# Optimization experiments

Measured on AMD Instinct MI355X. Metric: run time of the kernel, lower is better.

## Reference

```python
import jax, jax.numpy as jnp
import numpy as np

B, S, L, F = 32, 48, 64, 256


def setup_inputs() -> dict:
    key = jax.random.key(0)
    ks = jax.random.split(key, 7)
    return {
        "features": jax.random.normal(ks[0], (B, S, L, F), dtype=jnp.float32),
        "src_locs": jax.random.normal(ks[1], (B, L, 2), dtype=jnp.float32),
        "tar_locs": jax.random.normal(ks[2], (B, 2), dtype=jnp.float32),
        "W1": jax.random.normal(ks[3], (F, F), dtype=jnp.float32) * (1.0 / np.sqrt(F)),
        "b1": jax.random.normal(ks[4], (F,), dtype=jnp.float32) * 0.02,
        "W2": jax.random.normal(ks[5], (F, 1), dtype=jnp.float32) * (1.0 / np.sqrt(F)),
        "b2": jax.random.normal(ks[6], (1,), dtype=jnp.float32) * 0.02,
    }


def reference(features, src_locs, tar_locs, W1, b1, W2, b2):
    # features: (B, S, L, F); src_locs: (B, L, 2); tar_locs: (B, 2)
    # MLP score: Linear(F,F) + ReLU + Linear(F,1) + ReLU -> (B, S, L, 1)
    attn = jax.nn.relu(jnp.einsum('bslf,fg->bslg', features, W1) + b1)
    attn = jax.nn.relu(jnp.einsum('bslf,fo->bslo', attn, W2) + b2)  # (B,S,L,1)
    # inverse-distance weights over stations: (B, L)
    dists = jnp.sqrt(jnp.sum((src_locs - tar_locs[:, None, :]) ** 2, axis=-1))
    inv_dists = 1.0 / dists  # (B, L)
    # broadcast to (B, 1, L, 1), softmax over src_length axis (axis=2)
    attn_scores = jax.nn.softmax(attn * inv_dists[:, None, :, None], axis=2)
    # weighted sum over stations -> (B, S, F)
    return jnp.sum(features * attn_scores, axis=2)
```

## Files before the change

kernel.cpp:

```cpp
#include <hip/hip_runtime.h>
#include <hip/hip_fp16.h>
#include <math.h>

typedef _Float16 half8 __attribute__((ext_vector_type(8)));
typedef float floatx4 __attribute__((ext_vector_type(4)));

#define BB 32
#define SS 48
#define LL 64
#define FF 256

#define WAVE_BARRIER() do {                                          \
    asm volatile("s_waitcnt lgkmcnt(0)" ::: "memory");               \
    __builtin_amdgcn_s_barrier();                                    \
    asm volatile("" ::: "memory");                                   \
} while (0)

#define ISSUE_FENCE() asm volatile("" ::: "memory")

template <int CTRL>
__device__ __forceinline__ float dpp_add(float x) {
    int y = __builtin_amdgcn_update_dpp(0, __float_as_int(x), CTRL, 0xF, 0xF, true);
    return x + __int_as_float(y);
}
template <int CTRL>
__device__ __forceinline__ float dpp_max(float x) {
    int y = __builtin_amdgcn_update_dpp(0, __float_as_int(x), CTRL, 0xF, 0xF, true);
    return fmaxf(x, __int_as_float(y));
}
__device__ __forceinline__ float row16_sum(float x) {
    x = dpp_add<0xB1>(x);
    x = dpp_add<0x4E>(x);
    x = dpp_add<0x124>(x);
    x = dpp_add<0x128>(x);
    return x;
}
__device__ __forceinline__ float row16_max(float x) {
    x = dpp_max<0xB1>(x);
    x = dpp_max<0x4E>(x);
    x = dpp_max<0x124>(x);
    x = dpp_max<0x128>(x);
    return x;
}

__global__ __launch_bounds__(256) void prep_w(const float* __restrict__ W1,
                                              _Float16* __restrict__ whi) {
    int idx = blockIdx.x * 256 + threadIdx.x;
    int j    = idx & 7;
    int lane = (idx >> 3) & 63;
    int nt   = (idx >> 9) & 15;
    int kt   = idx >> 13;
    int k = kt * 32 + ((lane >> 4) & 3) * 8 + j;
    int n = nt * 16 + (lane & 15);
    whi[idx] = (_Float16)W1[k * FF + n];
}

__global__ __launch_bounds__(512, 6) void ida_mfma(
    const float* __restrict__ features,
    const float* __restrict__ src_locs,
    const float* __restrict__ tar_locs,
    const _Float16* __restrict__ whi,
    const float* __restrict__ b1,
    const float* __restrict__ W2,
    const float* __restrict__ b2,
    float* __restrict__ out)
{
    __shared__ _Float16 Ahi[16384];
    __shared__ float SP[8 * LL];

    const int t    = threadIdx.x;
    const int w    = t >> 6;
    const int lane = t & 63;
    const int quad = lane >> 4;
    const int l16  = lane & 15;
    const int bs   = blockIdx.x;
    const int b    = bs / SS;

    const float* Xg = features + (size_t)bs * (LL * FF);

    float sx = src_locs[(b * LL + lane) * 2 + 0];
    float sy = src_locs[(b * LL + lane) * 2 + 1];
    float tx = tar_locs[b * 2 + 0];
    float ty = tar_locs[b * 2 + 1];
    float b2v = b2[0];
    float b1v[2], w2v[2];
    #pragma unroll
    for (int ntl = 0; ntl < 2; ++ntl) {
        int n = (w * 2 + ntl) * 16 + l16;
        b1v[ntl] = b1[n];
        w2v[ntl] = W2[n];
    }
    ISSUE_FENCE();

    float4 araw[8];
    #pragma unroll
    for (int it = 0; it < 4; ++it) {
        int G   = it * 8 + w;
        int row = (G >> 3) * 16 + l16;
        int cb  = (G & 7) * 32 + quad * 8;
        const float4* p = (const float4*)(Xg + row * FF + cb);
        araw[2 * it + 0] = p[0];
        araw[2 * it + 1] = p[1];
    }
    ISSUE_FENCE();

    half8 bh[2], nbh[2];
    #pragma unroll
    for (int ntl = 0; ntl < 2; ++ntl) {
        size_t off = ((size_t)(0 * 16 + (w * 2 + ntl)) * 64 + lane) * 8;
        bh[ntl] = *((const half8*)(whi + off));
    }
    ISSUE_FENCE();

    #pragma unroll
    for (int it = 0; it < 4; ++it) {
        int G = it * 8 + w;
        float4 x0 = araw[2 * it + 0], x1 = araw[2 * it + 1];
        float xs[8] = {x0.x, x0.y, x0.z, x0.w, x1.x, x1.y, x1.z, x1.w};
        half8 hi;
        #pragma unroll
        for (int j = 0; j < 8; ++j) hi[j] = (_Float16)xs[j];
        *((half8*)&Ahi[(G * 64 + lane) * 8]) = hi;
    }

    WAVE_BARRIER();

    floatx4 acc[4][2] = {};

    #pragma unroll
    for (int kt = 0; kt < 8; ++kt) {
        if (kt < 7) {
            #pragma unroll
            for (int ntl = 0; ntl < 2; ++ntl) {
                size_t off = ((size_t)((kt + 1) * 16 + (w * 2 + ntl)) * 64 + lane) * 8;
                nbh[ntl] = *((const half8*)(whi + off));
            }
        }
        #pragma unroll
        for (int mt = 0; mt < 4; ++mt) {
            half8 ahi = *((half8*)&Ahi[((mt * 8 + kt) * 64 + lane) * 8]);
            #pragma unroll
            for (int ntl = 0; ntl < 2; ++ntl)
                acc[mt][ntl] = __builtin_amdgcn_mfma_f32_16x16x32_f16(ahi, bh[ntl], acc[mt][ntl], 0, 0, 0);
        }
        if (kt < 7) { bh[0] = nbh[0]; bh[1] = nbh[1]; }
    }

    #pragma unroll
    for (int mt = 0; mt < 4; ++mt) {
        #pragma unroll
        for (int r = 0; r < 4; ++r) {
            float p = 0.f;
            #pragma unroll
            for (int ntl = 0; ntl < 2; ++ntl) {
                float h = fmaxf(acc[mt][ntl][r] + b1v[ntl], 0.f);
                p = fmaf(h, w2v[ntl], p);
            }
            p = row16_sum(p);
            if (l16 == 0) SP[w * LL + mt * 16 + quad * 4 + r] = p;
        }
    }

    WAVE_BARRIER();

    float s = SP[0 * LL + lane] + SP[1 * LL + lane] + SP[2 * LL + lane] + SP[3 * LL + lane]
            + SP[4 * LL + lane] + SP[5 * LL + lane] + SP[6 * LL + lane] + SP[7 * LL + lane] + b2v;
    float score = fmaxf(s, 0.f);
    float dxv = sx - tx, dyv = sy - ty;
    float inv_d = 1.0f / sqrtf(dxv * dxv + dyv * dyv);
    float logit = score * inv_d;
    float m = row16_max(logit);
    m = fmaxf(m, __shfl_xor(m, 16));
    m = fmaxf(m, __shfl_xor(m, 32));
    float e = __expf(logit - m);
    float se = row16_sum(e);
    se += __shfl_xor(se, 16);
    se += __shfl_xor(se, 32);
    float wgt = e / se;

    float o8[8] = {0.f, 0.f, 0.f, 0.f, 0.f, 0.f, 0.f, 0.f};
    #pragma unroll
    for (int it = 0; it < 4; ++it) {
        float wr = __shfl(wgt, it * 16 + l16);
        half8 hv = *((half8*)&Ahi[((it * 8 + w) * 64 + lane) * 8]);
        #pragma unroll
        for (int j = 0; j < 8; ++j)
            o8[j] = fmaf((float)hv[j], wr, o8[j]);
    }
    #pragma unroll
    for (int j = 0; j < 8; ++j)
        o8[j] = row16_sum(o8[j]);
    if (l16 == 0) {
        float* op = out + (size_t)bs * FF + w * 32 + quad * 8;
        float4 s0 = {o8[0], o8[1], o8[2], o8[3]};
        float4 s1 = {o8[4], o8[5], o8[6], o8[7]};
        *((float4*)op) = s0;
        *((float4*)(op + 4)) = s1;
    }
}

extern "C" void kernel_launch(void* const* d_in, const int* in_sizes, int n_in,
                              void* d_out, int out_size, void* d_ws, size_t ws_size,
                              hipStream_t stream) {
    const float* features = (const float*)d_in[0];
    const float* src_locs = (const float*)d_in[1];
    const float* tar_locs = (const float*)d_in[2];
    const float* W1       = (const float*)d_in[3];
    const float* b1       = (const float*)d_in[4];
    const float* W2       = (const float*)d_in[5];
    const float* b2       = (const float*)d_in[6];
    float* out = (float*)d_out;

    _Float16* whi = (_Float16*)d_ws;

    prep_w<<<dim3(FF * FF / 256), dim3(256), 0, stream>>>(W1, whi);
    ida_mfma<<<dim3(BB * SS), dim3(512), 0, stream>>>(
        features, src_locs, tar_locs, whi, b1, W2, b2, out);
}
```

Baseline: 171.9 us.

## Process three slices per block with register prefetch and double-buffered LDS

Each block now handles three consecutive (b,s) slices instead of one, shrinking the grid by a factor of three. While the MFMA stage of the current slice runs, the next slice's features are loaded into registers, and a two-entry LDS buffer lets the conversion of the next slice proceed without waiting for the current one to be fully consumed. The W1 fragment prefetch becomes a three-deep ring that loads two k-tiles ahead. The cost is twice the LDS per block, a lower occupancy hint, and fewer blocks to spread across the CUs.

```diff
diff --git a/kernel.cpp b/kernel.cpp
--- a/kernel.cpp
+++ b/kernel.cpp
@@ -9,6 +9,8 @@
 #define SS 48
 #define LL 64
 #define FF 256
+#define NSLICE 3
+#define NBLK ((BB * SS) / NSLICE)
 
 #define WAVE_BARRIER() do {                                          \
     asm volatile("s_waitcnt lgkmcnt(0)" ::: "memory");               \
@@ -55,7 +57,7 @@
     whi[idx] = (_Float16)W1[k * FF + n];
 }
 
-__global__ __launch_bounds__(512, 6) void ida_mfma(
+__global__ __launch_bounds__(512, 4) void ida_mfma(
     const float* __restrict__ features,
     const float* __restrict__ src_locs,
     const float* __restrict__ tar_locs,
@@ -65,7 +67,7 @@
     const float* __restrict__ b2,
     float* __restrict__ out)
 {
-    __shared__ _Float16 Ahi[16384];
+    __shared__ _Float16 Ahi[2][16384];
     __shared__ float SP[8 * LL];
 
     const int t    = threadIdx.x;
@@ -73,16 +75,8 @@
     const int lane = t & 63;
     const int quad = lane >> 4;
     const int l16  = lane & 15;
-    const int bs   = blockIdx.x;
-    const int b    = bs / SS;
-
-    const float* Xg = features + (size_t)bs * (LL * FF);
-
-    float sx = src_locs[(b * LL + lane) * 2 + 0];
-    float sy = src_locs[(b * LL + lane) * 2 + 1];
-    float tx = tar_locs[b * 2 + 0];
-    float ty = tar_locs[b * 2 + 1];
-    float b2v = b2[0];
+    const int g    = blockIdx.x;
+
     float b1v[2], w2v[2];
     #pragma unroll
     for (int ntl = 0; ntl < 2; ++ntl) {
@@ -93,109 +87,132 @@
     ISSUE_FENCE();
 
     float4 araw[8];
-    #pragma unroll
-    for (int it = 0; it < 4; ++it) {
-        int G   = it * 8 + w;
-        int row = (G >> 3) * 16 + l16;
-        int cb  = (G & 7) * 32 + quad * 8;
-        const float4* p = (const float4*)(Xg + row * FF + cb);
-        araw[2 * it + 0] = p[0];
-        araw[2 * it + 1] = p[1];
+    {
+        const float* Xg0 = features + (size_t)(g * NSLICE) * (LL * FF);
+        #pragma unroll
+        for (int it = 0; it < 4; ++it) {
+            const float4* p = (const float4*)(Xg0 + (it * 16 + l16) * FF + w * 32 + quad * 8);
+            araw[2 * it + 0] = p[0];
+            araw[2 * it + 1] = p[1];
+        }
     }
     ISSUE_FENCE();
 
-    half8 bh[2], nbh[2];
     #pragma unroll
-    for (int ntl = 0; ntl < 2; ++ntl) {
-        size_t off = ((size_t)(0 * 16 + (w * 2 + ntl)) * 64 + lane) * 8;
-        bh[ntl] = *((const half8*)(whi + off));
-    }
-    ISSUE_FENCE();
-
-    #pragma unroll
-    for (int it = 0; it < 4; ++it) {
-        int G = it * 8 + w;
-        float4 x0 = araw[2 * it + 0], x1 = araw[2 * it + 1];
-        float xs[8] = {x0.x, x0.y, x0.z, x0.w, x1.x, x1.y, x1.z, x1.w};
-        half8 hi;
-        #pragma unroll
-        for (int j = 0; j < 8; ++j) hi[j] = (_Float16)xs[j];
-        *((half8*)&Ahi[(G * 64 + lane) * 8]) = hi;
-    }
-
-    WAVE_BARRIER();
-
-    floatx4 acc[4][2] = {};
-
-    #pragma unroll
-    for (int kt = 0; kt < 8; ++kt) {
-        if (kt < 7) {
-            #pragma unroll
-            for (int ntl = 0; ntl < 2; ++ntl) {
-                size_t off = ((size_t)((kt + 1) * 16 + (w * 2 + ntl)) * 64 + lane) * 8;
-                nbh[ntl] = *((const half8*)(whi + off));
-            }
-        }
+    for (int i = 0; i < NSLICE; ++i) {
+        const int bs = g * NSLICE + i;
+        const int b  = bs / SS;
+        _Float16* Abuf = &Ahi[i & 1][0];
+        const float* Xg = features + (size_t)bs * (LL * FF);
+
+        float sx = src_locs[(b * LL + lane) * 2 + 0];
+        float sy = src_locs[(b * LL + lane) * 2 + 1];
+        float tx = tar_locs[b * 2 + 0];
+        float ty = tar_locs[b * 2 + 1];
+        float b2v = b2[0];
+        ISSUE_FENCE();
+
+        #pragma unroll
+        for (int it = 0; it < 4; ++it) {
+            int G = it * 8 + w;
+            float4 x0 = araw[2 * it + 0], x1 = araw[2 * it + 1];
+            float xs[8] = {x0.x, x0.y, x0.z, x0.w, x1.x, x1.y, x1.z, x1.w};
+            half8 hi;
+            #pragma unroll
+            for (int j = 0; j < 8; ++j) hi[j] = (_Float16)xs[j];
+            *((half8*)&Abuf[(G * 64 + lane) * 8]) = hi;
+        }
+
+        half8 bq[3][2];
+        #pragma unroll
+        for (int c = 0; c < 2; ++c)
+            #pragma unroll
+            for (int ntl = 0; ntl < 2; ++ntl)
+                bq[c][ntl] = *((const half8*)(whi + ((size_t)(c * 16 + (w * 2 + ntl)) * 64 + lane) * 8));
+        ISSUE_FENCE();
+
+        WAVE_BARRIER();
+
+        floatx4 acc[4][2] = {};
+
+        #pragma unroll
+        for (int kt = 0; kt < 8; ++kt) {
+            if (kt < 6) {
+                #pragma unroll
+                for (int ntl = 0; ntl < 2; ++ntl)
+                    bq[(kt + 2) % 3][ntl] = *((const half8*)(whi + ((size_t)((kt + 2) * 16 + (w * 2 + ntl)) * 64 + lane) * 8));
+            }
+            #pragma unroll
+            for (int mt = 0; mt < 4; ++mt) {
+                half8 ahi = *((half8*)&Abuf[((mt * 8 + kt) * 64 + lane) * 8]);
+                #pragma unroll
+                for (int ntl = 0; ntl < 2; ++ntl)
+                    acc[mt][ntl] = __builtin_amdgcn_mfma_f32_16x16x32_f16(ahi, bq[kt % 3][ntl], acc[mt][ntl], 0, 0, 0);
+            }
+        }
+
+        if (i + 1 < NSLICE) {
+            const float* Xgn = features + (size_t)(bs + 1) * (LL * FF);
+            #pragma unroll
+            for (int it = 0; it < 4; ++it) {
+                const float4* p = (const float4*)(Xgn + (it * 16 + l16) * FF + w * 32 + quad * 8);
+                araw[2 * it + 0] = p[0];
+                araw[2 * it + 1] = p[1];
+            }
+            ISSUE_FENCE();
+        }
+
         #pragma unroll
         for (int mt = 0; mt < 4; ++mt) {
-            half8 ahi = *((half8*)&Ahi[((mt * 8 + kt) * 64 + lane) * 8]);
-            #pragma unroll
-            for (int ntl = 0; ntl < 2; ++ntl)
-                acc[mt][ntl] = __builtin_amdgcn_mfma_f32_16x16x32_f16(ahi, bh[ntl], acc[mt][ntl], 0, 0, 0);
-        }
-        if (kt < 7) { bh[0] = nbh[0]; bh[1] = nbh[1]; }
-    }
-
-    #pragma unroll
-    for (int mt = 0; mt < 4; ++mt) {
-        #pragma unroll
-        for (int r = 0; r < 4; ++r) {
-            float p = 0.f;
-            #pragma unroll
-            for (int ntl = 0; ntl < 2; ++ntl) {
-                float h = fmaxf(acc[mt][ntl][r] + b1v[ntl], 0.f);
-                p = fmaf(h, w2v[ntl], p);
-            }
-            p = row16_sum(p);
-            if (l16 == 0) SP[w * LL + mt * 16 + quad * 4 + r] = p;
-        }
-    }
-
-    WAVE_BARRIER();
-
-    float s = SP[0 * LL + lane] + SP[1 * LL + lane] + SP[2 * LL + lane] + SP[3 * LL + lane]
-            + SP[4 * LL + lane] + SP[5 * LL + lane] + SP[6 * LL + lane] + SP[7 * LL + lane] + b2v;
-    float score = fmaxf(s, 0.f);
-    float dxv = sx - tx, dyv = sy - ty;
-    float inv_d = 1.0f / sqrtf(dxv * dxv + dyv * dyv);
-    float logit = score * inv_d;
-    float m = row16_max(logit);
-    m = fmaxf(m, __shfl_xor(m, 16));
-    m = fmaxf(m, __shfl_xor(m, 32));
-    float e = __expf(logit - m);
-    float se = row16_sum(e);
-    se += __shfl_xor(se, 16);
-    se += __shfl_xor(se, 32);
-    float wgt = e / se;
-
-    float o8[8] = {0.f, 0.f, 0.f, 0.f, 0.f, 0.f, 0.f, 0.f};
-    #pragma unroll
-    for (int it = 0; it < 4; ++it) {
-        float wr = __shfl(wgt, it * 16 + l16);
-        half8 hv = *((half8*)&Ahi[((it * 8 + w) * 64 + lane) * 8]);
+            #pragma unroll
+            for (int r = 0; r < 4; ++r) {
+                float p = 0.f;
+                #pragma unroll
+                for (int ntl = 0; ntl < 2; ++ntl) {
+                    float h = fmaxf(acc[mt][ntl][r] + b1v[ntl], 0.f);
+                    p = fmaf(h, w2v[ntl], p);
+                }
+                p = row16_sum(p);
+                if (l16 == 0) SP[w * LL + mt * 16 + quad * 4 + r] = p;
+            }
+        }
+
+        WAVE_BARRIER();
+
+        float s = SP[0 * LL + lane] + SP[1 * LL + lane] + SP[2 * LL + lane] + SP[3 * LL + lane]
+                + SP[4 * LL + lane] + SP[5 * LL + lane] + SP[6 * LL + lane] + SP[7 * LL + lane] + b2v;
+        float score = fmaxf(s, 0.f);
+        float dxv = sx - tx, dyv = sy - ty;
+        float inv_d = 1.0f / sqrtf(dxv * dxv + dyv * dyv);
+        float logit = score * inv_d;
+        float m = row16_max(logit);
+        m = fmaxf(m, __shfl_xor(m, 16));
+        m = fmaxf(m, __shfl_xor(m, 32));
+        float e = __expf(logit - m);
+        float se = row16_sum(e);
+        se += __shfl_xor(se, 16);
+        se += __shfl_xor(se, 32);
+        float wgt = e / se;
+
+        float o8[8] = {0.f, 0.f, 0.f, 0.f, 0.f, 0.f, 0.f, 0.f};
+        #pragma unroll
+        for (int it = 0; it < 4; ++it) {
+            float wr = __shfl(wgt, it * 16 + l16);
+            half8 hv = *((half8*)&Abuf[((it * 8 + w) * 64 + lane) * 8]);
+            #pragma unroll
+            for (int j = 0; j < 8; ++j)
+                o8[j] = fmaf((float)hv[j], wr, o8[j]);
+        }
         #pragma unroll
         for (int j = 0; j < 8; ++j)
-            o8[j] = fmaf((float)hv[j], wr, o8[j]);
-    }
-    #pragma unroll
-    for (int j = 0; j < 8; ++j)
-        o8[j] = row16_sum(o8[j]);
-    if (l16 == 0) {
-        float* op = out + (size_t)bs * FF + w * 32 + quad * 8;
-        float4 s0 = {o8[0], o8[1], o8[2], o8[3]};
-        float4 s1 = {o8[4], o8[5], o8[6], o8[7]};
-        *((float4*)op) = s0;
-        *((float4*)(op + 4)) = s1;
+            o8[j] = row16_sum(o8[j]);
+        if (l16 == 0) {
+            float* op = out + (size_t)bs * FF + w * 32 + quad * 8;
+            float4 s0 = {o8[0], o8[1], o8[2], o8[3]};
+            float4 s1 = {o8[4], o8[5], o8[6], o8[7]};
+            *((float4*)op) = s0;
+            *((float4*)(op + 4)) = s1;
+        }
     }
 }
 
@@ -214,6 +231,6 @@
     _Float16* whi = (_Float16*)d_ws;
 
     prep_w<<<dim3(FF * FF / 256), dim3(256), 0, stream>>>(W1, whi);
-    ida_mfma<<<dim3(BB * SS), dim3(512), 0, stream>>>(
+    ida_mfma<<<dim3(NBLK), dim3(512), 0, stream>>>(
         features, src_locs, tar_locs, whi, b1, W2, b2, out);
 }
```

Result: faster. 164.4 us (-4.3%).
